# Optimization experiments

Measured on AMD Instinct MI355X. Metric: run time of the kernel, lower is better.

The kernel has to match this reference:

```python
import jax, jax.numpy as jnp
import numpy as np

B, S, D, H = 8, 2048, 768, 768


def setup_inputs() -> dict:
    key = jax.random.key(0)
    kx, kq, kk, kv = jax.random.split(key, 4)
    scale = 1.0 / np.sqrt(D)
    return {
        "x": jax.random.normal(kx, (B, S, D), dtype=jnp.float32),
        "Wq": jax.random.normal(kq, (D, H), dtype=jnp.float32) * scale,
        "Wk": jax.random.normal(kk, (D, H), dtype=jnp.float32) * scale,
        "Wv": jax.random.normal(kv, (D, H), dtype=jnp.float32) * scale,
    }


def reference(x, Wq, Wk, Wv):
    # Dense(use_bias=False) projections
    q = jnp.einsum("bsd,dh->bsh", x, Wq)
    k = jnp.einsum("bsd,dh->bsh", x, Wk)
    v = jnp.einsum("bsd,dh->bsh", x, Wv)
    S_len = x.shape[-2]
    # NOTE: source does NOT scale by 1/sqrt(head_size)
    scores = jnp.einsum("bqh,bkh->bqk", q, k)  # [B, S, S]
    tril = jnp.tril(jnp.ones((S_len, S_len), dtype=jnp.float32))
    scores = jnp.where(tril == 0, -jnp.inf, scores)
    attn = jax.nn.softmax(scores, axis=-1)
    # Dropout rate is 0.0 in Config -> identity
    return jnp.einsum("bqk,bkh->bqh", attn, v)
```

## Files before the change

kernel.cpp:

```cpp
#include <hip/hip_runtime.h>

typedef unsigned short u16;
typedef _Float16 f16;
typedef float  f32x4  __attribute__((ext_vector_type(4)));
typedef unsigned short u16x4 __attribute__((ext_vector_type(4)));
typedef f16    f16x8  __attribute__((ext_vector_type(8)));

__device__ __forceinline__ u16 f2h(float f) {
  f16 h = (f16)f;
  return __builtin_bit_cast(u16, h);
}

#define BARRIER()                          \
  do {                                     \
    asm volatile("" ::: "memory");         \
    __builtin_amdgcn_s_barrier();          \
    asm volatile("" ::: "memory");         \
  } while (0)

#define GLL16(g, l)                                                              \
  __builtin_amdgcn_global_load_lds(                                              \
      (const __attribute__((address_space(1))) unsigned int*)(g),                \
      (__attribute__((address_space(3))) unsigned int*)(l), 16, 0, 0)

__global__ __launch_bounds__(256) void prep_kernel(
    const float* __restrict__ x, const float* __restrict__ Wq,
    const float* __restrict__ Wk, const float* __restrict__ Wv,
    u16* __restrict__ xf, u16* __restrict__ wq16,
    u16* __restrict__ wk16, u16* __restrict__ wvt16) {
  const int bid = blockIdx.x, tid = threadIdx.x;
  if (bid < 13440) {
    const float* src;
    u16* dst;
    int i;
    if (bid < 12288) { src = x;  dst = xf;   i = bid * 256 + tid; }
    else if (bid < 12864) { src = Wq; dst = wq16; i = (bid - 12288) * 256 + tid; }
    else { src = Wk; dst = wk16; i = (bid - 12864) * 256 + tid; }
    f32x4 v = ((const f32x4*)src)[i];
    u16x4 h;
#pragma unroll
    for (int j = 0; j < 4; ++j) h[j] = f2h(v[j]);
    ((u16x4*)dst)[i] = h;
  } else {
    int i = (bid - 13440) * 256 + tid;
    int h = i / 768, d = i % 768;
    wvt16[i] = f2h(Wv[d * 768 + h]);
  }
}

template <int EPI, int CAUSAL, int KROW, int BN>
__device__ __forceinline__ void gemm_body(
    u16* __restrict__ lds,
    const u16* __restrict__ pA, const u16* __restrict__ pB,
    void* __restrict__ Cv, size_t cbase,
    int K, int lda, int ldb, int ldc, int ti, int tj) {
  constexpr int BSZ = BN * 32;
  u16* As = lds;
  u16* Bs = lds + 2 * 4096;

  const int t = threadIdx.x, w = t >> 6, l = t & 63;
  const int wr = w >> 1, wc = w & 1;
  const int lr = l & 15, lk = l >> 4;
  constexpr int NI = BN / 32;
  constexpr int LPS = 2 + BN / 64;

  const int srow = t >> 2;
  const int sk8 = ((t & 3) ^ ((srow >> 1) & 3)) * 8;
  const int ck = ((lk ^ ((lr >> 1) & 3)) << 3);

  const size_t aOff0 = (size_t)(ti * 128 + srow) * lda + sk8;
  const size_t aOff1 = (size_t)(ti * 128 + 64 + srow) * lda + sk8;
  const size_t bOff0 = (size_t)(tj * BN + srow) * ldb + sk8;
  const size_t bOff1 = (size_t)(tj * BN + 64 + srow) * ldb + sk8;

  const int Keff = KROW ? (ti + 1) * 128 : K;
  const int nsteps = Keff >> 5;

  auto stage = [&](int bu, int kk) {
    const int kb = kk * 32;
    GLL16(pA + aOff0 + kb, As + bu * 4096 + w * 512);
    GLL16(pA + aOff1 + kb, As + bu * 4096 + 2048 + w * 512);
    GLL16(pB + bOff0 + kb, Bs + bu * BSZ + w * 512);
    if constexpr (BN == 128) GLL16(pB + bOff1 + kb, Bs + bu * BSZ + 2048 + w * 512);
  };

  f32x4 acc[4][NI] = {};

  stage(0, 0);
  int buf = 0;
  for (int kk = 0; kk < nsteps; ++kk) {
    if (kk + 1 < nsteps) {
      stage(buf ^ 1, kk + 1);
      if constexpr (LPS == 4) asm volatile("s_waitcnt vmcnt(4)" ::: "memory");
      else                    asm volatile("s_waitcnt vmcnt(3)" ::: "memory");
    } else {
      asm volatile("s_waitcnt vmcnt(0)" ::: "memory");
    }
    BARRIER();

    f16x8 ah[4], bh[NI];
#pragma unroll
    for (int mi = 0; mi < 4; ++mi) {
      const int ae = buf * 4096 + (wr * 64 + mi * 16 + lr) * 32 + ck;
      ah[mi] = *(const f16x8*)&As[ae];
    }
#pragma unroll
    for (int ni = 0; ni < NI; ++ni) {
      const int be = buf * BSZ + (wc * (BN / 2) + ni * 16 + lr) * 32 + ck;
      bh[ni] = *(const f16x8*)&Bs[be];
    }
#pragma unroll
    for (int mi = 0; mi < 4; ++mi)
#pragma unroll
      for (int ni = 0; ni < NI; ++ni)
        acc[mi][ni] = __builtin_amdgcn_mfma_f32_16x16x32_f16(ah[mi], bh[ni], acc[mi][ni], 0, 0, 0);
    BARRIER();
    buf ^= 1;
  }

#pragma unroll
  for (int mi = 0; mi < 4; ++mi)
#pragma unroll
    for (int ni = 0; ni < NI; ++ni)
#pragma unroll
      for (int r = 0; r < 4; ++r) {
        const int row = ti * 128 + wr * 64 + mi * 16 + lk * 4 + r;
        const int col = tj * BN + wc * (BN / 2) + ni * 16 + lr;
        float v = acc[mi][ni][r];
        if (CAUSAL && col > row) v = -1e30f;
        const size_t idx = cbase + (size_t)row * ldc + col;
        if (EPI == 0) ((float*)Cv)[idx] = v;
        else          ((u16*)Cv)[idx] = f2h(v);
      }
}

template <int EPI, int CAUSAL, int KROW, int BN>
__global__ __launch_bounds__(256, 4) void gemm_k(
    const u16* __restrict__ A, long sAb, const u16* __restrict__ B, long sBb,
    void* __restrict__ Cv, long sCb,
    int K, int lda, int ldb, int ldc, int gx, int gy) {
  __shared__ __align__(16) u16 lds[2 * (4096 + BN * 32)];
  const int nwg = gridDim.x;
  const int orig = blockIdx.x;
  const int q8 = nwg >> 3, r8 = nwg & 7;
  const int xcd = orig & 7, pos = orig >> 3;
  const int wgid = (xcd < r8 ? xcd * (q8 + 1) : r8 * (q8 + 1) + (xcd - r8) * q8) + pos;
  const int tj = wgid % gx;
  const int rest = wgid / gx;
  const int ti = rest % gy;
  const int zb = rest / gy;
  if (CAUSAL && tj > ti) return;
  gemm_body<EPI, CAUSAL, KROW, BN>(
      lds, A + (size_t)zb * sAb, B + (size_t)zb * sBb,
      Cv, (size_t)zb * sCb, K, lda, ldb, ldc, ti, tj);
}

__global__ __launch_bounds__(256, 4) void proj_kernel(
    const u16* __restrict__ xf, const u16* __restrict__ mt16,
    const u16* __restrict__ wvt16,
    u16* __restrict__ qf, u16* __restrict__ vtf) {
  __shared__ __align__(16) u16 lds[2 * (4096 + 4096)];
  const int orig = blockIdx.x;
  const int wgid = (orig & 7) * 96 + (orig >> 3);
#pragma unroll
  for (int j = 0; j < 2; ++j) {
    const int job = wgid * 2 + j;
    const int sidx = job / 12, sub = job % 12;
    if (sub < 6) {
      gemm_body<2, 0, 0, 128>(lds, xf, mt16, qf, 0, 768, 768, 768, 768, sidx, sub);
    } else {
      gemm_body<2, 0, 0, 128>(lds, wvt16, xf, vtf, 0, 768, 768, 768, 16384, sub - 6, sidx);
    }
  }
}

__global__ __launch_bounds__(256) void softmax_kernel(const float* __restrict__ S,
                                                      u16* __restrict__ P,
                                                      long sSb, long sPb) {
  const int wid = blockIdx.x * 4 + (threadIdx.x >> 6);
  const int l = threadIdx.x & 63;
  const int zb = wid >> 11;
  const int i = wid & 2047;
  const float* row = S + (size_t)zb * sSb + (size_t)i * 2048;
  u16* prow = P + (size_t)zb * sPb + (size_t)i * 2048;
  const int Tend = ((i >> 7) + 1) << 7;
  const int nch = (Tend + 255) >> 8;

  f32x4 vb[8];
  float mx = -3e38f;
  for (int c = 0; c < nch; ++c) {
    const int j = c * 256 + l * 4;
    f32x4 v;
    if (j < Tend) v = *(const f32x4*)(row + j);
    else { v[0] = v[1] = v[2] = v[3] = -3e38f; }
    vb[c] = v;
    mx = fmaxf(mx, fmaxf(fmaxf(v[0], v[1]), fmaxf(v[2], v[3])));
  }
#pragma unroll
  for (int s = 32; s; s >>= 1) mx = fmaxf(mx, __shfl_xor(mx, s));

  float sum = 0.f;
  for (int c = 0; c < nch; ++c) {
    f32x4 v = vb[c];
#pragma unroll
    for (int j = 0; j < 4; ++j) {
      float e = expf(v[j] - mx);
      v[j] = e;
      sum += e;
    }
    vb[c] = v;
  }
#pragma unroll
  for (int s = 32; s; s >>= 1) sum += __shfl_xor(sum, s);
  const float inv = 1.f / sum;

  for (int c = 0; c < nch; ++c) {
    const int j = c * 256 + l * 4;
    if (j < Tend) {
      f32x4 v = vb[c];
      u16x4 o;
#pragma unroll
      for (int q = 0; q < 4; ++q) o[q] = f2h(v[q] * inv);
      *(u16x4*)(prow + j) = o;
    }
  }
}

extern "C" void kernel_launch(void* const* d_in, const int* in_sizes, int n_in,
                              void* d_out, int out_size, void* d_ws, size_t ws_size,
                              hipStream_t stream) {
  const float* x  = (const float*)d_in[0];
  const float* Wq = (const float*)d_in[1];
  const float* Wk = (const float*)d_in[2];
  const float* Wv = (const float*)d_in[3];
  float* out = (float*)d_out;

  const int S = 2048, D = 768;
  const size_t ND = (size_t)8 * S * D;
  const size_t NW = (size_t)D * D;

  char* ws = (char*)d_ws;
  size_t off = 0;
  auto alloc = [&](size_t bytes) { size_t o = off; off = (off + bytes + 255) & ~(size_t)255; return o; };

  u16* xf   = (u16*)(ws + alloc(ND * 2));
  u16* qf   = (u16*)(ws + alloc(ND * 2));
  u16* vtf  = (u16*)(ws + alloc(ND * 2));
  u16* wq16 = (u16*)(ws + alloc(NW * 2));
  u16* wk16 = (u16*)(ws + alloc(NW * 2));
  u16* wvt16= (u16*)(ws + alloc(NW * 2));
  u16* mt16 = (u16*)(ws + alloc(NW * 2));
  const size_t fixed = off;

  const size_t perBatch = (size_t)S * S * 4 + (size_t)S * S * 2 + 512;
  int g = 0;
  for (int cand = 8; cand >= 1; cand >>= 1)
    if (fixed + (size_t)cand * perBatch <= ws_size) { g = cand; break; }
  if (!g) return;

  float* sc = (float*)(ws + alloc((size_t)g * S * S * 4));
  u16*   P  = (u16*)(ws + alloc((size_t)g * S * S * 2));

  prep_kernel<<<15744, 256, 0, stream>>>(x, Wq, Wk, Wv, xf, wq16, wk16, wvt16);

  gemm_k<2, 0, 0, 64><<<72, 256, 0, stream>>>(
      wk16, 0, wq16, 0, mt16, 0, 768, 768, 768, 768, 12, 6);

  proj_kernel<<<768, 256, 0, stream>>>(xf, mt16, wvt16, qf, vtf);

  for (int b0 = 0; b0 < 8; b0 += g) {
    gemm_k<0, 1, 0, 128><<<16 * 16 * g, 256, 0, stream>>>(
        qf + (size_t)b0 * S * D, (long)S * D,
        xf + (size_t)b0 * S * D, (long)S * D,
        sc, (long)S * S, 768, 768, 768, 2048, 16, 16);

    softmax_kernel<<<g * 512, 256, 0, stream>>>(sc, P, (long)S * S, (long)S * S);

    gemm_k<0, 0, 1, 128><<<6 * 16 * g, 256, 0, stream>>>(
        P, (long)S * S,
        vtf + (size_t)b0 * S, (long)S,
        out + (size_t)b0 * S * D, (long)S * D,
        2048, 2048, 16384, 768, 6, 16);
  }
}
```

Measured before the change: 227.9 us.

## Generalize GEMM tile shape and retile projection and PV kernels with balanced scheduling

The GEMM body is parameterized over BM, BN and pipeline depth. The projection kernel now does one 64x256 Q tile and one 128x128 V^T tile per workgroup instead of two 128x128 jobs. The P·V GEMM moves to a dedicated kernel using 64x256 tiles, with causal row tiles interleaved from both ends so short and long K ranges pair up across the grid. This aims to improve load balance and per-tile reuse, at the cost of more LDS per block and lower occupancy (launch bounds 3).

```diff
diff --git a/kernel.cpp b/kernel.cpp
--- a/kernel.cpp
+++ b/kernel.cpp
@@ -17,6 +17,16 @@
     __builtin_amdgcn_s_barrier();          \
     asm volatile("" ::: "memory");         \
   } while (0)
+
+template <int N> __device__ __forceinline__ void vmwait() {
+  if constexpr (N == 0)       asm volatile("s_waitcnt vmcnt(0)" ::: "memory");
+  else if constexpr (N == 3)  asm volatile("s_waitcnt vmcnt(3)" ::: "memory");
+  else if constexpr (N == 4)  asm volatile("s_waitcnt vmcnt(4)" ::: "memory");
+  else if constexpr (N == 5)  asm volatile("s_waitcnt vmcnt(5)" ::: "memory");
+  else if constexpr (N == 6)  asm volatile("s_waitcnt vmcnt(6)" ::: "memory");
+  else if constexpr (N == 8)  asm volatile("s_waitcnt vmcnt(8)" ::: "memory");
+  else if constexpr (N == 10) asm volatile("s_waitcnt vmcnt(10)" ::: "memory");
+}
 
 #define GLL16(g, l)                                                              \
   __builtin_amdgcn_global_load_lds(                                              \
@@ -48,60 +58,63 @@
   }
 }
 
-template <int EPI, int CAUSAL, int KROW, int BN>
+template <int EPI, int CAUSAL, int KROW, int BM, int BN, int DEPTH>
 __device__ __forceinline__ void gemm_body(
     u16* __restrict__ lds,
     const u16* __restrict__ pA, const u16* __restrict__ pB,
     void* __restrict__ Cv, size_t cbase,
     int K, int lda, int ldb, int ldc, int ti, int tj) {
+  constexpr int ASZ = BM * 32;
   constexpr int BSZ = BN * 32;
   u16* As = lds;
-  u16* Bs = lds + 2 * 4096;
+  u16* Bs = lds + DEPTH * ASZ;
 
   const int t = threadIdx.x, w = t >> 6, l = t & 63;
   const int wr = w >> 1, wc = w & 1;
   const int lr = l & 15, lk = l >> 4;
+  constexpr int MI = BM / 32;
   constexpr int NI = BN / 32;
-  constexpr int LPS = 2 + BN / 64;
+  constexpr int LPS = BM / 64 + BN / 64;
 
   const int srow = t >> 2;
   const int sk8 = ((t & 3) ^ ((srow >> 1) & 3)) * 8;
   const int ck = ((lk ^ ((lr >> 1) & 3)) << 3);
 
-  const size_t aOff0 = (size_t)(ti * 128 + srow) * lda + sk8;
-  const size_t aOff1 = (size_t)(ti * 128 + 64 + srow) * lda + sk8;
-  const size_t bOff0 = (size_t)(tj * BN + srow) * ldb + sk8;
-  const size_t bOff1 = (size_t)(tj * BN + 64 + srow) * ldb + sk8;
-
-  const int Keff = KROW ? (ti + 1) * 128 : K;
+  const int Keff = KROW ? (ti + 1) * BM : K;
   const int nsteps = Keff >> 5;
 
   auto stage = [&](int bu, int kk) {
     const int kb = kk * 32;
-    GLL16(pA + aOff0 + kb, As + bu * 4096 + w * 512);
-    GLL16(pA + aOff1 + kb, As + bu * 4096 + 2048 + w * 512);
-    GLL16(pB + bOff0 + kb, Bs + bu * BSZ + w * 512);
-    if constexpr (BN == 128) GLL16(pB + bOff1 + kb, Bs + bu * BSZ + 2048 + w * 512);
+#pragma unroll
+    for (int s = 0; s < BM / 64; ++s)
+      GLL16(pA + (size_t)(ti * BM + s * 64 + srow) * lda + sk8 + kb,
+            As + bu * ASZ + s * 2048 + w * 512);
+#pragma unroll
+    for (int s = 0; s < BN / 64; ++s)
+      GLL16(pB + (size_t)(tj * BN + s * 64 + srow) * ldb + sk8 + kb,
+            Bs + bu * BSZ + s * 2048 + w * 512);
   };
 
-  f32x4 acc[4][NI] = {};
+  f32x4 acc[MI][NI] = {};
 
   stage(0, 0);
-  int buf = 0;
+  if constexpr (DEPTH == 3) { if (nsteps > 1) stage(1, 1); }
   for (int kk = 0; kk < nsteps; ++kk) {
-    if (kk + 1 < nsteps) {
-      stage(buf ^ 1, kk + 1);
-      if constexpr (LPS == 4) asm volatile("s_waitcnt vmcnt(4)" ::: "memory");
-      else                    asm volatile("s_waitcnt vmcnt(3)" ::: "memory");
+    const int buf = kk % DEPTH;
+    if constexpr (DEPTH == 2) {
+      if (kk + 1 < nsteps) { stage((kk + 1) % 2, kk + 1); vmwait<LPS>(); }
+      else vmwait<0>();
     } else {
-      asm volatile("s_waitcnt vmcnt(0)" ::: "memory");
+      if (kk + 2 < nsteps) { stage((kk + 2) % 3, kk + 2); vmwait<2 * LPS>(); }
+      else if (kk + 1 < nsteps) vmwait<LPS>();
+      else vmwait<0>();
     }
     BARRIER();
 
-    f16x8 ah[4], bh[NI];
-#pragma unroll
-    for (int mi = 0; mi < 4; ++mi) {
-      const int ae = buf * 4096 + (wr * 64 + mi * 16 + lr) * 32 + ck;
+    f16x8 ah[MI], bh[NI];
+#pragma unroll
+    for (int mi = 0; mi < MI; ++mi) {
+      const int ae = buf * ASZ + (wr * (BM / 2) + mi * 16 + lr) * 32 + ck;
       ah[mi] = *(const f16x8*)&As[ae];
     }
 #pragma unroll
@@ -110,21 +123,20 @@
       bh[ni] = *(const f16x8*)&Bs[be];
     }
 #pragma unroll
-    for (int mi = 0; mi < 4; ++mi)
+    for (int mi = 0; mi < MI; ++mi)
 #pragma unroll
       for (int ni = 0; ni < NI; ++ni)
         acc[mi][ni] = __builtin_amdgcn_mfma_f32_16x16x32_f16(ah[mi], bh[ni], acc[mi][ni], 0, 0, 0);
     BARRIER();
-    buf ^= 1;
-  }
-
-#pragma unroll
-  for (int mi = 0; mi < 4; ++mi)
+  }
+
+#pragma unroll
+  for (int mi = 0; mi < MI; ++mi)
 #pragma unroll
     for (int ni = 0; ni < NI; ++ni)
 #pragma unroll
       for (int r = 0; r < 4; ++r) {
-        const int row = ti * 128 + wr * 64 + mi * 16 + lk * 4 + r;
+        const int row = ti * BM + wr * (BM / 2) + mi * 16 + lk * 4 + r;
         const int col = tj * BN + wc * (BN / 2) + ni * 16 + lr;
         float v = acc[mi][ni][r];
         if (CAUSAL && col > row) v = -1e30f;
@@ -134,12 +146,12 @@
       }
 }
 
-template <int EPI, int CAUSAL, int KROW, int BN>
-__global__ __launch_bounds__(256, 4) void gemm_k(
+template <int EPI, int CAUSAL, int BM, int BN, int DEPTH, int MINW>
+__global__ __launch_bounds__(256, MINW) void gemm_k(
     const u16* __restrict__ A, long sAb, const u16* __restrict__ B, long sBb,
     void* __restrict__ Cv, long sCb,
     int K, int lda, int ldb, int ldc, int gx, int gy) {
-  __shared__ __align__(16) u16 lds[2 * (4096 + BN * 32)];
+  __shared__ __align__(16) u16 lds[DEPTH * (BM * 32 + BN * 32)];
   const int nwg = gridDim.x;
   const int orig = blockIdx.x;
   const int q8 = nwg >> 3, r8 = nwg & 7;
@@ -150,28 +162,39 @@
   const int ti = rest % gy;
   const int zb = rest / gy;
   if (CAUSAL && tj > ti) return;
-  gemm_body<EPI, CAUSAL, KROW, BN>(
+  gemm_body<EPI, CAUSAL, 0, BM, BN, DEPTH>(
       lds, A + (size_t)zb * sAb, B + (size_t)zb * sBb,
       Cv, (size_t)zb * sCb, K, lda, ldb, ldc, ti, tj);
 }
 
-__global__ __launch_bounds__(256, 4) void proj_kernel(
+__global__ __launch_bounds__(256, 3) void proj_kernel(
     const u16* __restrict__ xf, const u16* __restrict__ mt16,
     const u16* __restrict__ wvt16,
     u16* __restrict__ qf, u16* __restrict__ vtf) {
-  __shared__ __align__(16) u16 lds[2 * (4096 + 4096)];
+  __shared__ __align__(16) u16 lds[20480];
   const int orig = blockIdx.x;
   const int wgid = (orig & 7) * 96 + (orig >> 3);
-#pragma unroll
-  for (int j = 0; j < 2; ++j) {
-    const int job = wgid * 2 + j;
-    const int sidx = job / 12, sub = job % 12;
-    if (sub < 6) {
-      gemm_body<2, 0, 0, 128>(lds, xf, mt16, qf, 0, 768, 768, 768, 768, sidx, sub);
-    } else {
-      gemm_body<2, 0, 0, 128>(lds, wvt16, xf, vtf, 0, 768, 768, 768, 16384, sub - 6, sidx);
-    }
-  }
+  gemm_body<2, 0, 0, 64, 256, 2>(lds, xf, mt16, qf, 0,
+                                 768, 768, 768, 768, wgid / 3, wgid % 3);
+  gemm_body<2, 0, 0, 128, 128, 2>(lds, wvt16, xf, vtf, 0,
+                                  768, 768, 768, 16384, wgid % 6, wgid / 6);
+}
+
+__global__ __launch_bounds__(256, 3) void pv_kernel(
+    const u16* __restrict__ P, long sPb,
+    const u16* __restrict__ vt,
+    float* __restrict__ out, long sOb) {
+  __shared__ __align__(16) u16 lds[20480];
+  const int orig = blockIdx.x;
+  const int nwg = gridDim.x;
+  const int wgid = (orig & 7) * (nwg >> 3) + (orig >> 3);
+  const int tj = wgid % 3;
+  const int s5 = (wgid / 3) % 32;
+  const int zb = wgid / 96;
+  const int ti = (s5 & 1) ? (s5 >> 1) : (31 - (s5 >> 1));
+  gemm_body<0, 0, 1, 64, 256, 2>(
+      lds, P + (size_t)zb * sPb, vt + (size_t)zb * 2048,
+      out, (size_t)zb * sOb, 2048, 2048, 16384, 768, ti, tj);
 }
 
 __global__ __launch_bounds__(256) void softmax_kernel(const float* __restrict__ S,
@@ -263,23 +286,21 @@
 
   prep_kernel<<<15744, 256, 0, stream>>>(x, Wq, Wk, Wv, xf, wq16, wk16, wvt16);
 
-  gemm_k<2, 0, 0, 64><<<72, 256, 0, stream>>>(
+  gemm_k<2, 0, 128, 64, 2, 4><<<72, 256, 0, stream>>>(
       wk16, 0, wq16, 0, mt16, 0, 768, 768, 768, 768, 12, 6);
 
   proj_kernel<<<768, 256, 0, stream>>>(xf, mt16, wvt16, qf, vtf);
 
   for (int b0 = 0; b0 < 8; b0 += g) {
-    gemm_k<0, 1, 0, 128><<<16 * 16 * g, 256, 0, stream>>>(
+    gemm_k<0, 1, 128, 128, 2, 4><<<16 * 16 * g, 256, 0, stream>>>(
         qf + (size_t)b0 * S * D, (long)S * D,
         xf + (size_t)b0 * S * D, (long)S * D,
         sc, (long)S * S, 768, 768, 768, 2048, 16, 16);
 
     softmax_kernel<<<g * 512, 256, 0, stream>>>(sc, P, (long)S * S, (long)S * S);
 
-    gemm_k<0, 0, 1, 128><<<6 * 16 * g, 256, 0, stream>>>(
-        P, (long)S * S,
-        vtf + (size_t)b0 * S, (long)S,
-        out + (size_t)b0 * S * D, (long)S * D,
-        2048, 2048, 16384, 768, 6, 16);
-  }
-}
+    pv_kernel<<<96 * g, 256, 0, stream>>>(
+        P, (long)S * S, vtf + (size_t)b0 * S,
+        out + (size_t)b0 * S * D, (long)S * D);
+  }
+}
```

Result: slower. 242.6 us (+6.4%).
